# Performance work log

Measured on AMD Instinct MI355X. Metric: run time of the kernel, lower is better.

## Reference

```python
import jax, jax.numpy as jnp
import numpy as np

NUM_HEADS = 8
D_MODEL = 256
DIM = D_MODEL // NUM_HEADS  # 32
EPS = 1e-6


def _proj(x, W, b):
    # Conv1d with kernel_size=1 == channel-mixing matmul over length axis
    return jnp.einsum('oi,bil->bol', W, x) + b[None, :, None]


def _linear_attention(q, k, v):
    # q,k,v: [B, dim, heads, L]
    q = jax.nn.elu(q) + 1.0
    k = jax.nn.elu(k) + 1.0
    L = v.shape[3]
    v = v / L
    # KV: [B, dim_v, dim_k, heads]
    KV = jnp.einsum('bdhm,bqhm->bqdh', k, v)
    # Z: [B, heads, L]
    Z = 1.0 / (jnp.einsum('bdhm,bdh->bhm', q, k.sum(3)) + EPS)
    # out: [B, dim, heads, L]
    return jnp.einsum('bdhm,bqdh,bhm->bqhm', q, KV, Z) * L


def setup_inputs() -> dict:
    key = jax.random.key(0)
    ks = jax.random.split(key, 11)
    B, L = 8, 4096
    s = 0.05
    return {
        'query': jax.random.normal(ks[0], (B, D_MODEL, L), dtype=jnp.float32),
        'key':   jax.random.normal(ks[1], (B, D_MODEL, L), dtype=jnp.float32),
        'value': jax.random.normal(ks[2], (B, D_MODEL, L), dtype=jnp.float32),
        'Wq': jax.random.normal(ks[3], (D_MODEL, D_MODEL), dtype=jnp.float32) * s,
        'bq': jnp.zeros((D_MODEL,), dtype=jnp.float32),
        'Wk': jax.random.normal(ks[4], (D_MODEL, D_MODEL), dtype=jnp.float32) * s,
        'bk': jnp.zeros((D_MODEL,), dtype=jnp.float32),
        'Wv': jax.random.normal(ks[5], (D_MODEL, D_MODEL), dtype=jnp.float32) * s,
        'bv': jnp.zeros((D_MODEL,), dtype=jnp.float32),
        'Wm': jax.random.normal(ks[6], (D_MODEL, D_MODEL), dtype=jnp.float32) * s,
        'bm': jnp.zeros((D_MODEL,), dtype=jnp.float32),
    }


def reference(query, key, value, Wq, bq, Wk, bk, Wv, bv, Wm, bm):
    B = query.shape[0]
    q = _proj(query, Wq, bq).reshape(B, DIM, NUM_HEADS, -1)
    k = _proj(key,   Wk, bk).reshape(B, DIM, NUM_HEADS, -1)
    v = _proj(value, Wv, bv).reshape(B, DIM, NUM_HEADS, -1)
    x = _linear_attention(q, k, v)           # [B, dim, heads, L]
    x = x.reshape(B, D_MODEL, -1)            # merge heads back to channels
    return jnp.einsum('oi,bil->bol', Wm, x) + bm[None, :, None]
```

## Files before the change

### kernel.cpp

```cpp
#include <hip/hip_runtime.h>
#include <math.h>

#define D_MODEL 256
#define NHEADS 8
#define HDIM 32
#define BATCH 8
#define SEQL 4096
#define EPS 1e-6f

typedef _Float16 f16;
typedef _Float16 f16x4 __attribute__((ext_vector_type(4)));
typedef _Float16 f16x8 __attribute__((ext_vector_type(8)));
typedef float f32x4 __attribute__((ext_vector_type(4)));

__device__ __forceinline__ float elu1(float x) {
    return x > 0.f ? x + 1.f : __expf(x);
}

__global__ void prep_kernel(const float* __restrict__ Wq, const float* __restrict__ Wk,
                            const float* __restrict__ Wv, const float* __restrict__ Wm,
                            const float* __restrict__ bq, const float* __restrict__ bk,
                            const float* __restrict__ bv,
                            f16* __restrict__ w16, float* __restrict__ bperm,
                            float* __restrict__ KVz) {
    const int bid = blockIdx.x;
    if (bid < 1024) {
        int idx = bid * 256 + threadIdx.x;
        int mat = idx >> 16, r = (idx >> 8) & 255, c = idx & 255;
        const float* W = (mat == 0) ? Wq : (mat == 1) ? Wk : (mat == 2) ? Wv : Wm;
        float v;
        if (mat < 3) v = W[(size_t)(((r & 31) << 3) + (r >> 5)) * 256 + c];
        else         v = W[(size_t)r * 256 + (((c & 31) << 3) + (c >> 5))];
        w16[idx] = (f16)v;
    } else if (bid == 1024) {
        int t = threadIdx.x;
        bperm[0 * 256 + t] = bq[((t & 31) << 3) + (t >> 5)];
        bperm[1 * 256 + t] = bk[((t & 31) << 3) + (t >> 5)];
        bperm[2 * 256 + t] = bv[((t & 31) << 3) + (t >> 5)];
    } else {
        int i = (bid - 1025) * 256 + threadIdx.x;
        KVz[i] = 0.f;
    }
}

#define BSTR 40
__global__ __launch_bounds__(256, 3) void gemm_stage1(
    const float* __restrict__ Xq, const float* __restrict__ Xk, const float* __restrict__ Xv,
    const f16* __restrict__ w16, const float* __restrict__ bperm,
    f16* __restrict__ yq, f16* __restrict__ yk, f16* __restrict__ yv) {
    __shared__ __align__(16) char smem[20480];
    f16* B0 = (f16*)smem;
    f16* B1 = (f16*)smem + 128 * BSTR;
    f16* Cb = (f16*)smem;

    const int z = blockIdx.z;
    const int which = z >> 3;
    const int b = z & 7;
    const float* X = (which == 0) ? Xq : (which == 1) ? Xk : Xv;
    const f16* W = w16 + which * 65536;
    f16* Y = (which == 0) ? yq : (which == 1) ? yk : yv;
    const float* bp = bperm + which * 256;

    const int l0 = blockIdx.x * 128;
    const int m0 = blockIdx.y * 128;
    const int tid = threadIdx.x;
    const int wave = tid >> 6, lane = tid & 63;
    const int wm = wave >> 1, wn = wave & 1;
    const int ln = lane & 15, quad = lane >> 4;
    const int bp8 = tid & 7;
    const int bg = tid >> 3;

    const float* Xbase = X + ((size_t)b * D_MODEL + 4 * bp8) * SEQL + l0 + 4 * bg;
    const f16* Wb[4];
#pragma unroll
    for (int mf = 0; mf < 4; ++mf)
        Wb[mf] = W + (size_t)(m0 + wm * 64 + mf * 16 + ln) * 256 + quad * 8;

    float4 xa[4], xb[4];
    f16x8 afc[4], afn[4];

#define LOADX(DST, K0) do { \
        const float* xb_ = Xbase + (size_t)(K0) * SEQL; \
        DST[0] = *(const float4*)(xb_ + 0 * SEQL); \
        DST[1] = *(const float4*)(xb_ + 1 * SEQL); \
        DST[2] = *(const float4*)(xb_ + 2 * SEQL); \
        DST[3] = *(const float4*)(xb_ + 3 * SEQL); \
    } while (0)

#define STOREB(SRC, BUF) do { \
        f16x4 w_; \
        w_[0] = (f16)SRC[0].x; w_[1] = (f16)SRC[1].x; w_[2] = (f16)SRC[2].x; w_[3] = (f16)SRC[3].x; \
        *(f16x4*)&BUF[(4 * bg + 0) * BSTR + 4 * bp8] = w_; \
        w_[0] = (f16)SRC[0].y; w_[1] = (f16)SRC[1].y; w_[2] = (f16)SRC[2].y; w_[3] = (f16)SRC[3].y; \
        *(f16x4*)&BUF[(4 * bg + 1) * BSTR + 4 * bp8] = w_; \
        w_[0] = (f16)SRC[0].z; w_[1] = (f16)SRC[1].z; w_[2] = (f16)SRC[2].z; w_[3] = (f16)SRC[3].z; \
        *(f16x4*)&BUF[(4 * bg + 2) * BSTR + 4 * bp8] = w_; \
        w_[0] = (f16)SRC[0].w; w_[1] = (f16)SRC[1].w; w_[2] = (f16)SRC[2].w; w_[3] = (f16)SRC[3].w; \
        *(f16x4*)&BUF[(4 * bg + 3) * BSTR + 4 * bp8] = w_; \
    } while (0)

    f32x4 acc[4][4];
#pragma unroll
    for (int mf = 0; mf < 4; ++mf)
#pragma unroll
        for (int nf = 0; nf < 4; ++nf)
#pragma unroll
            for (int r = 0; r < 4; ++r) acc[mf][nf][r] = 0.f;

    LOADX(xa, 0);
#pragma unroll
    for (int mf = 0; mf < 4; ++mf) afc[mf] = *(const f16x8*)(Wb[mf] + 0);

#pragma unroll
    for (int it = 0; it < 8; ++it) {
        const int k0 = it * 32;
        f16* buf = (it & 1) ? B1 : B0;
        if (it < 7) {
            if (it & 1) LOADX(xa, k0 + 32);
            else        LOADX(xb, k0 + 32);
        }
        if (it & 1) STOREB(xb, buf);
        else        STOREB(xa, buf);
        __syncthreads();
        if (it < 7) {
#pragma unroll
            for (int mf = 0; mf < 4; ++mf)
                afn[mf] = *(const f16x8*)(Wb[mf] + k0 + 32);
        }
        f16x8 bf[4];
#pragma unroll
        for (int nf = 0; nf < 4; ++nf)
            bf[nf] = *(const f16x8*)&buf[(wn * 64 + nf * 16 + ln) * BSTR + quad * 8];
#pragma unroll
        for (int mf = 0; mf < 4; ++mf)
#pragma unroll
            for (int nf = 0; nf < 4; ++nf)
                acc[mf][nf] = __builtin_amdgcn_mfma_f32_16x16x32_f16(afc[mf], bf[nf], acc[mf][nf], 0, 0, 0);
#pragma unroll
        for (int mf = 0; mf < 4; ++mf) afc[mf] = afn[mf];
    }

    float bv_[4][4];
#pragma unroll
    for (int mf = 0; mf < 4; ++mf)
#pragma unroll
        for (int r = 0; r < 4; ++r)
            bv_[mf][r] = bp[m0 + wm * 64 + mf * 16 + quad * 4 + r];
#pragma unroll
    for (int pass = 0; pass < 2; ++pass) {
        __syncthreads();
        if (wm == pass) {
#pragma unroll
            for (int mf = 0; mf < 4; ++mf)
#pragma unroll
                for (int nf = 0; nf < 4; ++nf) {
                    const int olocal = mf * 16 + quad * 4;
                    const int llocal = wn * 64 + nf * 16 + ln;
                    f16x4 w;
#pragma unroll
                    for (int r = 0; r < 4; ++r) w[r] = (f16)(acc[mf][nf][r] + bv_[mf][r]);
                    *(f16x4*)&Cb[llocal * 72 + olocal] = w;
                }
        }
        __syncthreads();
        const int l = tid >> 1, half = tid & 1;
        f16* yr = Y + ((size_t)(b * SEQL + l0 + l)) * 256 + m0 + pass * 64 + half * 32;
#pragma unroll
        for (int u = 0; u < 4; ++u)
            *(f16x8*)(yr + u * 8) = *(const f16x8*)&Cb[l * 72 + half * 32 + u * 8];
    }
}

__global__ __launch_bounds__(256) void kv_kernel(
    const f16* __restrict__ kp, const f16* __restrict__ vp,
    float* __restrict__ KV, float* __restrict__ ksum) {
    const int bh = blockIdx.y;
    const int b = bh >> 3, h = bh & 7;
    const int lbase = blockIdx.x * (SEQL / 16);
    __shared__ float ks[64][33];
    __shared__ float vs[64][33];
    const int t = threadIdx.x;
    const int lrow = t >> 2, seg = t & 3;
    const int kd = t & 31, qg = t >> 5;
    float a0 = 0.f, a1 = 0.f, a2 = 0.f, a3 = 0.f, ss = 0.f;
    for (int lc = 0; lc < SEQL / 16; lc += 64) {
        __syncthreads();
        const size_t off = ((size_t)(b * SEQL + lbase + lc + lrow)) * 256 + h * 32 + seg * 8;
        f16x8 k8 = *(const f16x8*)(kp + off);
        f16x8 v8 = *(const f16x8*)(vp + off);
#pragma unroll
        for (int j = 0; j < 8; ++j) {
            ks[lrow][seg * 8 + j] = elu1((float)k8[j]);
            vs[lrow][seg * 8 + j] = (float)v8[j];
        }
        __syncthreads();
#pragma unroll 8
        for (int li = 0; li < 64; ++li) {
            const float kk = ks[li][kd];
            ss += kk;
            a0 += kk * vs[li][qg * 4 + 0];
            a1 += kk * vs[li][qg * 4 + 1];
            a2 += kk * vs[li][qg * 4 + 2];
            a3 += kk * vs[li][qg * 4 + 3];
        }
    }
    float* KVb = KV + (size_t)(b * NHEADS + h) * HDIM * HDIM;
    atomicAdd(&KVb[(qg * 4 + 0) * HDIM + kd], a0);
    atomicAdd(&KVb[(qg * 4 + 1) * HDIM + kd], a1);
    atomicAdd(&KVb[(qg * 4 + 2) * HDIM + kd], a2);
    atomicAdd(&KVb[(qg * 4 + 3) * HDIM + kd], a3);
    if (qg == 0) atomicAdd(&ksum[(size_t)(b * NHEADS + h) * HDIM + kd], ss);
}

__global__ __launch_bounds__(256) void attn_out_kernel(
    const f16* __restrict__ qp, const float* __restrict__ KV,
    const float* __restrict__ ksum, const f16* __restrict__ wm16,
    const float* __restrict__ bm, float* __restrict__ out) {
    __shared__ __align__(16) f16 xs[64 * 264];
    __shared__ __align__(16) f16 Baug[8 * 48 * 40];
    __shared__ float dens[8][64];
    const int b = blockIdx.y;
    const int l0 = blockIdx.x * 64;
    const int t = threadIdx.x;
    const int wave = t >> 6, lane = t & 63;
    const int ln = lane & 15, quad = lane >> 4;

    {
        const int h = t >> 5, qd = t & 31;
        const float* kvp = KV + ((size_t)(b * NHEADS + h) * HDIM + qd) * HDIM;
        f16* dst = &Baug[(h * 48 + qd) * 40];
#pragma unroll
        for (int i = 0; i < 32; i += 4) {
            float4 a = *(const float4*)(kvp + i);
            f16x4 w4;
            w4[0] = (f16)a.x; w4[1] = (f16)a.y; w4[2] = (f16)a.z; w4[3] = (f16)a.w;
            *(f16x4*)(dst + i) = w4;
        }
        Baug[(h * 48 + 32) * 40 + qd] = (f16)ksum[(size_t)(b * NHEADS + h) * HDIM + qd];
    }
    {
        const int row = t & 63, cg = t >> 6;
        const f16* qr = qp + ((size_t)(b * SEQL + l0 + row)) * 256 + cg * 64;
        f16* dst = &xs[row * 264 + cg * 64];
#pragma unroll
        for (int u = 0; u < 64; u += 8) {
            f16x8 v = *(const f16x8*)(qr + u);
            f16x8 w;
#pragma unroll
            for (int j = 0; j < 8; ++j) w[j] = (f16)elu1((float)v[j]);
            *(f16x8*)(dst + u) = w;
        }
    }
    __syncthreads();
#pragma unroll
    for (int hh = 0; hh < 2; ++hh) {
        const int h = wave * 2 + hh;
        f16x8 a_s[4], b_s[3];
#pragma unroll
        for (int mf = 0; mf < 4; ++mf)
            a_s[mf] = *(const f16x8*)&xs[(mf * 16 + ln) * 264 + h * 32 + quad * 8];
#pragma unroll
        for (int nf = 0; nf < 3; ++nf)
            b_s[nf] = *(const f16x8*)&Baug[(h * 48 + nf * 16 + ln) * 40 + quad * 8];
        f32x4 C[4][3];
#pragma unroll
        for (int mf = 0; mf < 4; ++mf)
#pragma unroll
            for (int nf = 0; nf < 3; ++nf) {
#pragma unroll
                for (int r = 0; r < 4; ++r) C[mf][nf][r] = 0.f;
                C[mf][nf] = __builtin_amdgcn_mfma_f32_16x16x32_f16(a_s[mf], b_s[nf], C[mf][nf], 0, 0, 0);
            }
        if (ln == 0) {
#pragma unroll
            for (int mf = 0; mf < 4; ++mf)
#pragma unroll
                for (int r = 0; r < 4; ++r)
                    dens[h][mf * 16 + quad * 4 + r] = C[mf][2][r];
        }
        __syncthreads();
#pragma unroll
        for (int mf = 0; mf < 4; ++mf)
#pragma unroll
            for (int r = 0; r < 4; ++r) {
                const int l = mf * 16 + quad * 4 + r;
                const float rd = __builtin_amdgcn_rcpf(dens[h][l] + EPS);
#pragma unroll
                for (int nf = 0; nf < 2; ++nf)
                    xs[l * 264 + h * 32 + nf * 16 + ln] = (f16)(C[mf][nf][r] * rd);
            }
        __syncthreads();
    }
    f32x4 acc[4][4];
#pragma unroll
    for (int mf = 0; mf < 4; ++mf)
#pragma unroll
        for (int nf = 0; nf < 4; ++nf)
#pragma unroll
            for (int r = 0; r < 4; ++r) acc[mf][nf][r] = 0.f;
    const f16* Wb[4];
#pragma unroll
    for (int mf = 0; mf < 4; ++mf)
        Wb[mf] = wm16 + (size_t)(wave * 64 + mf * 16 + ln) * 256 + quad * 8;
    f16x8 afc[4], afn[4];
#pragma unroll
    for (int mf = 0; mf < 4; ++mf) afc[mf] = *(const f16x8*)(Wb[mf] + 0);
#pragma unroll
    for (int it = 0; it < 8; ++it) {
        const int k0 = it * 32;
        if (it < 7) {
#pragma unroll
            for (int mf = 0; mf < 4; ++mf) afn[mf] = *(const f16x8*)(Wb[mf] + k0 + 32);
        }
        f16x8 bf[4];
#pragma unroll
        for (int nf = 0; nf < 4; ++nf)
            bf[nf] = *(const f16x8*)&xs[(nf * 16 + ln) * 264 + k0 + quad * 8];
#pragma unroll
        for (int mf = 0; mf < 4; ++mf)
#pragma unroll
            for (int nf = 0; nf < 4; ++nf)
                acc[mf][nf] = __builtin_amdgcn_mfma_f32_16x16x32_f16(afc[mf], bf[nf], acc[mf][nf], 0, 0, 0);
#pragma unroll
        for (int mf = 0; mf < 4; ++mf) afc[mf] = afn[mf];
    }
#pragma unroll
    for (int mf = 0; mf < 4; ++mf) {
        const int o = wave * 64 + mf * 16 + quad * 4;
#pragma unroll
        for (int r = 0; r < 4; ++r) {
            const float bb = bm[o + r];
            float* op = out + ((size_t)(b * D_MODEL + o + r)) * SEQL + l0;
#pragma unroll
            for (int nf = 0; nf < 4; ++nf)
                op[nf * 16 + ln] = acc[mf][nf][r] + bb;
        }
    }
}

extern "C" void kernel_launch(void* const* d_in, const int* in_sizes, int n_in,
                              void* d_out, int out_size, void* d_ws, size_t ws_size,
                              hipStream_t stream) {
    const float* query = (const float*)d_in[0];
    const float* key_  = (const float*)d_in[1];
    const float* value = (const float*)d_in[2];
    const float* Wq = (const float*)d_in[3];
    const float* bq = (const float*)d_in[4];
    const float* Wk = (const float*)d_in[5];
    const float* bk = (const float*)d_in[6];
    const float* Wv = (const float*)d_in[7];
    const float* bv = (const float*)d_in[8];
    const float* Wm = (const float*)d_in[9];
    const float* bm = (const float*)d_in[10];

    char* w = (char*)d_ws;
    f16*   w16   = (f16*)w;
    float* bperm = (float*)(w + 524288);
    float* KV    = (float*)(w + 528384);
    float* ksum  = (float*)(w + 790528);
    f16*   qp    = (f16*)(w + 802816);
    f16*   kp    = qp + (size_t)BATCH * SEQL * 256;
    f16*   vp    = kp + (size_t)BATCH * SEQL * 256;

    prep_kernel<<<1289, 256, 0, stream>>>(Wq, Wk, Wv, Wm, bq, bk, bv, w16, bperm, KV);

    gemm_stage1<<<dim3(SEQL / 128, 2, 24), 256, 0, stream>>>(
        query, key_, value, w16, bperm, qp, kp, vp);

    kv_kernel<<<dim3(16, BATCH * NHEADS), 256, 0, stream>>>(kp, vp, KV, ksum);

    attn_out_kernel<<<dim3(SEQL / 64, BATCH), 256, 0, stream>>>(
        qp, KV, ksum, w16 + 3 * 65536, bm, (float*)d_out);
}
```

Baseline: 223.2 us.

## Compute KV and key sums with MFMA into per-split partials, drop atomics

Replaces the scalar FMA kv_kernel with an MFMA-based kernel that stages transposed elu(k) and v tiles in shared memory and computes KV and the key sum (via a row of ones appended to v) on matrix cores. Each of 8 sequence splits writes its own partial result, and attn_out sums the 8 partials when loading, so the zeroing pass in prep and the global atomics go away. The cost is extra partial-buffer reads in every attn_out block, and KV inputs are now in fp16 rather than fp32.

```diff
diff --git a/kernel.cpp b/kernel.cpp
--- a/kernel.cpp
+++ b/kernel.cpp
@@ -21,8 +21,7 @@
                             const float* __restrict__ Wv, const float* __restrict__ Wm,
                             const float* __restrict__ bq, const float* __restrict__ bk,
                             const float* __restrict__ bv,
-                            f16* __restrict__ w16, float* __restrict__ bperm,
-                            float* __restrict__ KVz) {
+                            f16* __restrict__ w16, float* __restrict__ bperm) {
     const int bid = blockIdx.x;
     if (bid < 1024) {
         int idx = bid * 256 + threadIdx.x;
@@ -32,14 +31,11 @@
         if (mat < 3) v = W[(size_t)(((r & 31) << 3) + (r >> 5)) * 256 + c];
         else         v = W[(size_t)r * 256 + (((c & 31) << 3) + (c >> 5))];
         w16[idx] = (f16)v;
-    } else if (bid == 1024) {
+    } else {
         int t = threadIdx.x;
         bperm[0 * 256 + t] = bq[((t & 31) << 3) + (t >> 5)];
         bperm[1 * 256 + t] = bk[((t & 31) << 3) + (t >> 5)];
         bperm[2 * 256 + t] = bv[((t & 31) << 3) + (t >> 5)];
-    } else {
-        int i = (bid - 1025) * 256 + threadIdx.x;
-        KVz[i] = 0.f;
     }
 }
 
@@ -169,52 +165,72 @@
         for (int u = 0; u < 4; ++u)
             *(f16x8*)(yr + u * 8) = *(const f16x8*)&Cb[l * 72 + half * 32 + u * 8];
     }
-}
-
-__global__ __launch_bounds__(256) void kv_kernel(
+#undef LOADX
+#undef STOREB
+}
+
+#define KVLP 66
+__global__ __launch_bounds__(256) void kv_mfma(
     const f16* __restrict__ kp, const f16* __restrict__ vp,
-    float* __restrict__ KV, float* __restrict__ ksum) {
+    float* __restrict__ KVpart, float* __restrict__ ksum_part) {
+    __shared__ __align__(16) f16 kT[32 * KVLP];
+    __shared__ __align__(16) f16 vT[48 * KVLP];
+    const int ls = blockIdx.x;
     const int bh = blockIdx.y;
     const int b = bh >> 3, h = bh & 7;
-    const int lbase = blockIdx.x * (SEQL / 16);
-    __shared__ float ks[64][33];
-    __shared__ float vs[64][33];
     const int t = threadIdx.x;
+    const int wave = t >> 6, lane = t & 63;
+    const int ln = lane & 15, quad = lane >> 4;
     const int lrow = t >> 2, seg = t & 3;
-    const int kd = t & 31, qg = t >> 5;
-    float a0 = 0.f, a1 = 0.f, a2 = 0.f, a3 = 0.f, ss = 0.f;
-    for (int lc = 0; lc < SEQL / 16; lc += 64) {
-        __syncthreads();
-        const size_t off = ((size_t)(b * SEQL + lbase + lc + lrow)) * 256 + h * 32 + seg * 8;
-        f16x8 k8 = *(const f16x8*)(kp + off);
-        f16x8 v8 = *(const f16x8*)(vp + off);
+
+    {
+        const int rr = 32 + (t >> 4), c0 = (t & 15) * 4;
+        f16x4 w;
+        const f16 one = (f16)1.f, zero = (f16)0.f;
+        w[0] = w[1] = w[2] = w[3] = (rr == 32) ? one : zero;
+        *(f16x4*)&vT[rr * KVLP + c0] = w;
+    }
+
+    const int tiP = wave >> 1, tjP = wave & 1;
+    f32x4 accP, accS;
+#pragma unroll
+    for (int r = 0; r < 4; ++r) { accP[r] = 0.f; accS[r] = 0.f; }
+
+    for (int ch = 0; ch < 8; ++ch) {
+        __syncthreads();
+        const size_t goff = ((size_t)(b * SEQL + ls * 512 + ch * 64 + lrow)) * 256 + h * 32 + seg * 8;
+        f16x8 k8 = *(const f16x8*)(kp + goff);
+        f16x8 v8 = *(const f16x8*)(vp + goff);
 #pragma unroll
         for (int j = 0; j < 8; ++j) {
-            ks[lrow][seg * 8 + j] = elu1((float)k8[j]);
-            vs[lrow][seg * 8 + j] = (float)v8[j];
-        }
-        __syncthreads();
-#pragma unroll 8
-        for (int li = 0; li < 64; ++li) {
-            const float kk = ks[li][kd];
-            ss += kk;
-            a0 += kk * vs[li][qg * 4 + 0];
-            a1 += kk * vs[li][qg * 4 + 1];
-            a2 += kk * vs[li][qg * 4 + 2];
-            a3 += kk * vs[li][qg * 4 + 3];
-        }
-    }
-    float* KVb = KV + (size_t)(b * NHEADS + h) * HDIM * HDIM;
-    atomicAdd(&KVb[(qg * 4 + 0) * HDIM + kd], a0);
-    atomicAdd(&KVb[(qg * 4 + 1) * HDIM + kd], a1);
-    atomicAdd(&KVb[(qg * 4 + 2) * HDIM + kd], a2);
-    atomicAdd(&KVb[(qg * 4 + 3) * HDIM + kd], a3);
-    if (qg == 0) atomicAdd(&ksum[(size_t)(b * NHEADS + h) * HDIM + kd], ss);
+            kT[(seg * 8 + j) * KVLP + lrow] = (f16)elu1((float)k8[j]);
+            vT[(seg * 8 + j) * KVLP + lrow] = v8[j];
+        }
+        __syncthreads();
+#pragma unroll
+        for (int ks = 0; ks < 2; ++ks) {
+            const int kc = ks * 32 + quad * 8;
+            f16x8 bP = *(const f16x8*)&kT[(tjP * 16 + ln) * KVLP + kc];
+            f16x8 aP = *(const f16x8*)&vT[(tiP * 16 + ln) * KVLP + kc];
+            accP = __builtin_amdgcn_mfma_f32_16x16x32_f16(aP, bP, accP, 0, 0, 0);
+            if (wave < 2) {
+                f16x8 aS = *(const f16x8*)&vT[(32 + ln) * KVLP + kc];
+                accS = __builtin_amdgcn_mfma_f32_16x16x32_f16(aS, bP, accS, 0, 0, 0);
+            }
+        }
+    }
+
+    float* KVp = KVpart + ((size_t)ls * 64 + bh) * 1024;
+#pragma unroll
+    for (int r = 0; r < 4; ++r)
+        KVp[(tiP * 16 + quad * 4 + r) * 32 + tjP * 16 + ln] = accP[r];
+    if (wave < 2 && quad == 0)
+        ksum_part[((size_t)ls * 64 + bh) * 32 + tjP * 16 + ln] = accS[0];
 }
 
 __global__ __launch_bounds__(256) void attn_out_kernel(
-    const f16* __restrict__ qp, const float* __restrict__ KV,
-    const float* __restrict__ ksum, const f16* __restrict__ wm16,
+    const f16* __restrict__ qp, const float* __restrict__ KVpart,
+    const float* __restrict__ ksum_part, const f16* __restrict__ wm16,
     const float* __restrict__ bm, float* __restrict__ out) {
     __shared__ __align__(16) f16 xs[64 * 264];
     __shared__ __align__(16) f16 Baug[8 * 48 * 40];
@@ -227,16 +243,25 @@
 
     {
         const int h = t >> 5, qd = t & 31;
-        const float* kvp = KV + ((size_t)(b * NHEADS + h) * HDIM + qd) * HDIM;
+        const float* kvp = KVpart + (size_t)(b * NHEADS + h) * 1024 + qd * 32;
         f16* dst = &Baug[(h * 48 + qd) * 40];
 #pragma unroll
         for (int i = 0; i < 32; i += 4) {
-            float4 a = *(const float4*)(kvp + i);
+            float ax = 0.f, ay = 0.f, az = 0.f, aw = 0.f;
+#pragma unroll
+            for (int s = 0; s < 8; ++s) {
+                float4 p = *(const float4*)(kvp + (size_t)s * 65536 + i);
+                ax += p.x; ay += p.y; az += p.z; aw += p.w;
+            }
             f16x4 w4;
-            w4[0] = (f16)a.x; w4[1] = (f16)a.y; w4[2] = (f16)a.z; w4[3] = (f16)a.w;
+            w4[0] = (f16)ax; w4[1] = (f16)ay; w4[2] = (f16)az; w4[3] = (f16)aw;
             *(f16x4*)(dst + i) = w4;
         }
-        Baug[(h * 48 + 32) * 40 + qd] = (f16)ksum[(size_t)(b * NHEADS + h) * HDIM + qd];
+        float ksv = 0.f;
+#pragma unroll
+        for (int s = 0; s < 8; ++s)
+            ksv += ksum_part[((size_t)s * 64 + b * NHEADS + h) * 32 + qd];
+        Baug[(h * 48 + 32) * 40 + qd] = (f16)ksv;
     }
     {
         const int row = t & 63, cg = t >> 6;
@@ -354,21 +379,21 @@
     const float* bm = (const float*)d_in[10];
 
     char* w = (char*)d_ws;
-    f16*   w16   = (f16*)w;
-    float* bperm = (float*)(w + 524288);
-    float* KV    = (float*)(w + 528384);
-    float* ksum  = (float*)(w + 790528);
-    f16*   qp    = (f16*)(w + 802816);
-    f16*   kp    = qp + (size_t)BATCH * SEQL * 256;
-    f16*   vp    = kp + (size_t)BATCH * SEQL * 256;
-
-    prep_kernel<<<1289, 256, 0, stream>>>(Wq, Wk, Wv, Wm, bq, bk, bv, w16, bperm, KV);
+    f16*   w16    = (f16*)w;
+    float* bperm  = (float*)(w + 524288);
+    float* KVpart = (float*)(w + 528384);
+    float* ksum_p = (float*)(w + 2625536);
+    f16*   qp     = (f16*)(w + 2691072);
+    f16*   kp     = qp + (size_t)BATCH * SEQL * 256;
+    f16*   vp     = kp + (size_t)BATCH * SEQL * 256;
+
+    prep_kernel<<<1025, 256, 0, stream>>>(Wq, Wk, Wv, Wm, bq, bk, bv, w16, bperm);
 
     gemm_stage1<<<dim3(SEQL / 128, 2, 24), 256, 0, stream>>>(
         query, key_, value, w16, bperm, qp, kp, vp);
 
-    kv_kernel<<<dim3(16, BATCH * NHEADS), 256, 0, stream>>>(kp, vp, KV, ksum);
+    kv_mfma<<<dim3(8, BATCH * NHEADS), 256, 0, stream>>>(kp, vp, KVpart, ksum_p);
 
     attn_out_kernel<<<dim3(SEQL / 64, BATCH), 256, 0, stream>>>(
-        qp, KV, ksum, w16 + 3 * 65536, bm, (float*)d_out);
-}
+        qp, KVpart, ksum_p, w16 + 3 * 65536, bm, (float*)d_out);
+}
```

After: 232.4 us. 4.1% more time.
